# Kernel tuning notes

Measured on AMD Instinct MI355X. Metric: run time of the kernel, lower is better.

## Reference

```python
import jax, jax.numpy as jnp
import numpy as np

C_IN = 512


def _rms(h, gamma):
    # F.normalize(x, dim=1) * sqrt(C) * gamma  (channel_first, h: [b, c, l])
    c = h.shape[1]
    n = jnp.sqrt(jnp.sum(h * h, axis=1, keepdims=True))
    return h / jnp.maximum(n, 1e-12) * (c ** 0.5) * gamma[None, :, None]


def _pw(w, b, h):
    # 1x1 conv == pointwise linear over channel dim; h: [b, c, l]
    return jnp.einsum('oc,bcl->bol', w, h) + b[None, :, None]


def setup_inputs() -> dict:
    key = jax.random.key(0)
    ks = jax.random.split(key, 10)
    B, C, T, H, W = 1, C_IN, 16, 32, 32
    inp = {'x': jax.random.normal(ks[0], (B, C, T, H, W), jnp.float32)}
    names = ['qs', 'ks', 'vs', 'ps', 'qt', 'kt', 'vt', 'pt']
    for i, n in enumerate(names):
        inp[n + '_w'] = jax.random.normal(ks[i + 1], (C, C), jnp.float32) * 0.02
        inp[n + '_b'] = jnp.zeros((C,), jnp.float32)
    inp['norm_s_gamma'] = jnp.ones((C,), jnp.float32)
    inp['norm_t_gamma'] = jnp.ones((C,), jnp.float32)
    inp['max_temporal_window'] = 8
    return inp


def reference(x, qs_w, qs_b, ks_w, ks_b, vs_w, vs_b, ps_w, ps_b,
              qt_w, qt_b, kt_w, kt_b, vt_w, vt_b, pt_w, pt_b,
              norm_s_gamma, norm_t_gamma, max_temporal_window):
    B, C, T, H, W = x.shape
    scale = C ** -0.5

    # ---- spatial attention: (b t) c (h w) ----
    xs = x.transpose(0, 2, 1, 3, 4).reshape(B * T, C, H * W)
    h = _rms(xs, norm_s_gamma)
    q = _pw(qs_w, qs_b, h)
    k = _pw(ks_w, ks_b, h)
    v = _pw(vs_w, vs_b, h)
    scores = jnp.einsum('bcl,bcm->blm', q, k) * scale  # [bt, HW, HW]
    attn = jax.nn.softmax(scores, axis=-1)
    o = jnp.einsum('bcm,blm->bcl', v, attn)
    xs = xs + _pw(ps_w, ps_b, o)
    x = xs.reshape(B, T, C, H, W).transpose(0, 2, 1, 3, 4)

    # ---- temporal attention: (b h w) c t, causal + bounded window ----
    xt = x.transpose(0, 3, 4, 1, 2).reshape(B * H * W, C, T)
    h = _rms(xt, norm_t_gamma)
    q = _pw(qt_w, qt_b, h)
    k = _pw(kt_w, kt_b, h)
    v = _pw(vt_w, vt_b, h)
    scores = jnp.einsum('bcl,bcm->blm', q, k) * scale  # [bhw, T, T]
    i = jnp.arange(T)[:, None]
    j = jnp.arange(T)[None, :]
    allowed = j <= i  # causal
    if max_temporal_window is not None and max_temporal_window > 0:
        allowed = allowed & (i - j < max_temporal_window)  # sliding window
    mask = jnp.where(allowed, 0.0, jnp.finfo(scores.dtype).min)
    attn = jax.nn.softmax(scores + mask[None], axis=-1)
    o = jnp.einsum('bcm,blm->bcl', v, attn)
    xt = xt + _pw(pt_w, pt_b, o)
    x = xt.reshape(B, H, W, C, T).transpose(0, 3, 4, 1, 2)
    return x
```

## Files before the change

kernel.cpp:

```cpp
#include <hip/hip_runtime.h>

typedef __attribute__((ext_vector_type(8))) short bf16x8;
typedef __attribute__((ext_vector_type(4))) float f32x4;

__device__ __forceinline__ short f2bf(float f) {
  union { float f; unsigned u; } a; a.f = f;
  unsigned r = a.u + 0x7fffu + ((a.u >> 16) & 1u);
  return (short)(r >> 16);
}
__device__ __forceinline__ float bf2f(short s) {
  union { unsigned u; float f; } a;
  a.u = ((unsigned)(unsigned short)s) << 16; return a.f;
}
__device__ __forceinline__ float blo(unsigned u) { union { unsigned u; float f; } a; a.u = u << 16; return a.f; }
__device__ __forceinline__ float bhi(unsigned u) { union { unsigned u; float f; } a; a.u = u & 0xffff0000u; return a.f; }
__device__ __forceinline__ unsigned packbf(float lo, float hi) {
  return (unsigned)(unsigned short)f2bf(lo) | ((unsigned)(unsigned short)f2bf(hi) << 16);
}
__device__ __forceinline__ void ldscp16(const void* g, void* l) {
  __builtin_amdgcn_global_load_lds((const __attribute__((address_space(1))) void*)g,
                                   (__attribute__((address_space(3))) void*)l, 16, 0, 0);
}
__device__ __forceinline__ void stv(float* p, float v) { *p = v; }
__device__ __forceinline__ void stv(short* p, float v) { *p = f2bf(v); }

__global__ __launch_bounds__(256) void setup_all(
    const float* __restrict__ w0, const float* __restrict__ w1,
    const float* __restrict__ w2, const float* __restrict__ w3,
    const float* __restrict__ w4, const float* __restrict__ w5,
    const float* __restrict__ w6, const float* __restrict__ w7,
    const float* __restrict__ g_s, const float* __restrict__ g_t,
    short* __restrict__ Wb, float* __restrict__ zs,
    const float* __restrict__ qs_b, const float* __restrict__ vs_b,
    const float* __restrict__ ps_b, const float* __restrict__ qt_b,
    const float* __restrict__ vt_b, const float* __restrict__ pt_b,
    float* __restrict__ bt_s, float* __restrict__ bt_t,
    float* __restrict__ wus, float* __restrict__ wut) {
  const int bid = blockIdx.x, tid = threadIdx.x;
  if (bid < 8192) {
    int idx = bid * 256 + tid;
    const float* ws[8] = {w0, w1, w2, w3, w4, w5, w6, w7};
    int wi = idx >> 18, loc = idx & 262143;
    int r = loc >> 9, q = loc & 511;
    float v, g;
    if (wi == 3 || wi == 7) { v = ws[wi][loc]; g = 1.f; }
    else {
      v = ws[wi][q * 512 + r];
      g = (wi <= 2) ? g_s[r] : g_t[r];
    }
    Wb[idx] = f2bf(v * g);
  } else if (bid < 8512) {
    zs[(bid - 8192) * 256 + tid] = 0.f;
  } else {
    const int w = tid >> 6, lane = tid & 63;
    const int b = (bid - 8512) * 4 + w;
    float s = 0.f;
    if (b < 1024) {
      const bool sp = b < 512;
      const float* W = sp ? w3 : w7;
      const float* vb = sp ? vs_b : vt_b;
      const int r = b & 511;
#pragma unroll
      for (int c = lane; c < 512; c += 64) s += W[r * 512 + c] * vb[c];
#pragma unroll
      for (int off = 32; off > 0; off >>= 1) s += __shfl_xor(s, off);
      if (lane == 0) (sp ? bt_s : bt_t)[r] = s + (sp ? ps_b : pt_b)[r];
    } else {
      const bool sp = b < 1536;
      const float* W = sp ? w1 : w5;
      const float* qb = sp ? qs_b : qt_b;
      const int c = b & 511;
#pragma unroll
      for (int o = lane; o < 512; o += 64) s += W[o * 512 + c] * qb[o];
#pragma unroll
      for (int off = 32; off > 0; off >>= 1) s += __shfl_xor(s, off);
      if (lane == 0)
        (sp ? wus : wut)[c] = s * (sp ? g_s[c] : g_t[c]);
    }
  }
}

__global__ __launch_bounds__(256) void txp_sumsq(
    const float* __restrict__ src, short* __restrict__ dst,
    short* __restrict__ xb, float* __restrict__ ss,
    const float* __restrict__ wu, float* __restrict__ us) {
  constexpr long N = 16384;
  __shared__ short T[64][66];
  __shared__ float part[16][16][4];
  __shared__ float part2[16][16][4];
  const int tid = threadIdx.x;
  const long n0 = (long)blockIdx.x * 64;
  const int c0 = blockIdx.y * 64;
  const int n4 = (tid & 15) * 4;
  float s0 = 0.f, s1 = 0.f, s2 = 0.f, s3 = 0.f;
  float u0 = 0.f, u1 = 0.f, u2 = 0.f, u3 = 0.f;
#pragma unroll
  for (int i = 0; i < 4; ++i) {
    int cl = i * 16 + (tid >> 4);
    float4 v = *(const float4*)&src[(long)(c0 + cl) * N + n0 + n4];
    float wc = wu[c0 + cl];
    s0 += v.x * v.x; s1 += v.y * v.y; s2 += v.z * v.z; s3 += v.w * v.w;
    u0 += wc * v.x; u1 += wc * v.y; u2 += wc * v.z; u3 += wc * v.w;
    short e0 = f2bf(v.x), e1 = f2bf(v.y), e2 = f2bf(v.z), e3 = f2bf(v.w);
    T[n4 + 0][cl] = e0; T[n4 + 1][cl] = e1;
    T[n4 + 2][cl] = e2; T[n4 + 3][cl] = e3;
    uint2 o;
    o.x = (unsigned)(unsigned short)e0 | ((unsigned)(unsigned short)e1 << 16);
    o.y = (unsigned)(unsigned short)e2 | ((unsigned)(unsigned short)e3 << 16);
    *(uint2*)&xb[(long)(c0 + cl) * N + n0 + n4] = o;
  }
  part[tid >> 4][tid & 15][0] = s0; part[tid >> 4][tid & 15][1] = s1;
  part[tid >> 4][tid & 15][2] = s2; part[tid >> 4][tid & 15][3] = s3;
  part2[tid >> 4][tid & 15][0] = u0; part2[tid >> 4][tid & 15][1] = u1;
  part2[tid >> 4][tid & 15][2] = u2; part2[tid >> 4][tid & 15][3] = u3;
  __syncthreads();
  if (tid < 64) {
    float s = 0.f, u = 0.f;
#pragma unroll
    for (int cg = 0; cg < 16; ++cg) {
      s += part[cg][tid >> 2][tid & 3];
      u += part2[cg][tid >> 2][tid & 3];
    }
    atomicAdd(&ss[n0 + tid], s);
    atomicAdd(&us[n0 + tid], u);
  }
#pragma unroll
  for (int p = 0; p < 4; ++p) {
    int nl = p * 16 + (tid >> 4);
    int cl = (tid & 15) * 4;
    uint2 o;
    o.x = (unsigned)(unsigned short)T[nl][cl] |
          ((unsigned)(unsigned short)T[nl][cl + 1] << 16);
    o.y = (unsigned)(unsigned short)T[nl][cl + 2] |
          ((unsigned)(unsigned short)T[nl][cl + 3] << 16);
    *(uint2*)&dst[(n0 + nl) * 512 + c0 + cl] = o;
  }
}

template <typename OutT, int BIAS_MODE, int SCALE_MODE, int RESID_MODE, int EPI,
          int BM = 128, int FOLD = 0, int BK = 64, int SWZ = 0>
__global__ __launch_bounds__(256, 4) void gemm_nt(
    const short* __restrict__ A, const short* __restrict__ B,
    OutT* __restrict__ D, const float* __restrict__ bias,
    const float* __restrict__ ssv, const float* __restrict__ uvec,
    float* __restrict__ rs, float* __restrict__ rs2,
    const float* __restrict__ wvec,
    const float* __restrict__ residf, const short* __restrict__ residb,
    int K, int lda, int ldb, int ldd,
    long aBatch, long bBatch, long dBatch, long sBatch, float scale) {
  constexpr int WR = BM / 64;
  constexpr int WC = 4 / WR;
  constexpr int NW = (128 / WC) / 16;
  constexpr int CH = BK / 8;
  constexpr int MSK = CH - 1;
  constexpr int RPR = 256 / CH;
  __shared__ short As[BM * BK];
  __shared__ short Bs[128 * BK];
  const int tid = threadIdx.x;

  int lin = blockIdx.x + gridDim.x * (blockIdx.y + gridDim.y * blockIdx.z);
  if (SWZ) {
    const int nwg = gridDim.x * gridDim.y * gridDim.z;
    const int q = nwg >> 3, r = nwg & 7;
    const int xcd = lin & 7, idx = lin >> 3;
    lin = (xcd < r ? xcd * (q + 1) : r * (q + 1) + (xcd - r) * q) + idx;
  }
  const int bx = lin % gridDim.x;
  const int t1 = lin / gridDim.x;
  const int by = t1 % gridDim.y;
  const int bz = t1 / gridDim.y;

  const long i0 = (long)bx * BM;
  const long j0 = (long)by * 128;
  long aOff, bOff;
  if (FOLD) {
    aOff = 262144L * (bz < 2 ? 3 + 4 * bz : 4 * (bz - 2));
    bOff = 262144L * (bz < 2 ? 2 + 4 * bz : 1 + 4 * (bz - 2));
  } else {
    aOff = bz * aBatch; bOff = bz * bBatch;
  }
  const short* Ab = A + aOff + i0 * lda;
  const short* Bb = B + bOff + j0 * ldb;
  const int srow = tid / CH, scol = tid & MSK;
  const int lane = tid & 63;
  const int waveid = tid >> 6;
  const int wr = (waveid / WC) * 64;
  const int wc = (waveid % WC) * 64;
  const int quad = lane >> 4, l15 = lane & 15;

  f32x4 acc[4][NW] = {};

  for (int k0 = 0; k0 < K; k0 += BK) {
    __syncthreads();
#pragma unroll
    for (int p = 0; p < BM / RPR; ++p) {
      int row = p * RPR + srow;
      int gc = (scol ^ (row & MSK)) << 3;
      ldscp16(Ab + (long)row * lda + k0 + gc, &As[p * 2048 + tid * 8]);
    }
#pragma unroll
    for (int p = 0; p < 128 / RPR; ++p) {
      int row = p * RPR + srow;
      int gc = (scol ^ (row & MSK)) << 3;
      ldscp16(Bb + (long)row * ldb + k0 + gc, &Bs[p * 2048 + tid * 8]);
    }
    __syncthreads();
#pragma unroll
    for (int kk = 0; kk < BK / 32; ++kk) {
      bf16x8 af[4], bfr[NW];
#pragma unroll
      for (int a = 0; a < 4; ++a) {
        int row = wr + a * 16 + l15;
        int g = kk * 4 + quad;
        af[a] = *(const bf16x8*)&As[row * BK + ((g ^ (row & MSK)) << 3)];
      }
#pragma unroll
      for (int b = 0; b < NW; ++b) {
        int row = wc + b * 16 + l15;
        int g = kk * 4 + quad;
        bfr[b] = *(const bf16x8*)&Bs[row * BK + ((g ^ (row & MSK)) << 3)];
      }
#pragma unroll
      for (int a = 0; a < 4; ++a)
#pragma unroll
        for (int b = 0; b < NW; ++b)
          acc[a][b] = __builtin_amdgcn_mfma_f32_16x16x32_bf16(af[a], bfr[b], acc[a][b], 0, 0, 0);
    }
  }

  const long Doff = bz * dBatch;
#pragma unroll
  for (int a = 0; a < 4; ++a) {
    const int rb = (int)i0 + wr + a * 16 + quad * 4;
    float rsc[4];
    if (SCALE_MODE == 1 || SCALE_MODE == 4) {
#pragma unroll
      for (int r = 0; r < 4; ++r)
        rsc[r] = 22.627416997969522f /
                 fmaxf(sqrtf(ssv[bz * sBatch + rb + r]), 1e-12f);
    }
    if (SCALE_MODE == 3) {
#pragma unroll
      for (int r = 0; r < 4; ++r)
        rsc[r] = 1.f / ssv[bz * sBatch + rb + r];
    }
    float rp1[4] = {0.f, 0.f, 0.f, 0.f};
    float rp2[4] = {0.f, 0.f, 0.f, 0.f};
#pragma unroll
    for (int b = 0; b < NW; ++b) {
      const int cc = (int)j0 + wc + b * 16 + l15;
      float csc = 1.f, uu = 0.f, wv = 0.f;
      if (SCALE_MODE == 2 || SCALE_MODE == 4)
        csc = 22.627416997969522f /
              fmaxf(sqrtf(ssv[bz * sBatch + cc]), 1e-12f);
      if (SCALE_MODE == 4) uu = uvec[bz * sBatch + cc];
      if (EPI == 3) wv = wvec[cc];
      uint2 rtv;
      if (RESID_MODE == 3)
        rtv = *(const uint2*)&residb[(long)cc * 512 + rb];
#pragma unroll
      for (int r = 0; r < 4; ++r) {
        float val;
        if (SCALE_MODE == 4) {
          val = __expf(scale * csc * (rsc[r] * acc[a][b][r] + uu));
          rp1[r] += val;
          val *= csc;
        } else {
          val = acc[a][b][r] * scale;
          if (SCALE_MODE == 1 || SCALE_MODE == 3) val *= rsc[r];
          if (SCALE_MODE == 2) val *= csc;
        }
        if (BIAS_MODE == 1) val += bias[rb + r];
        if (BIAS_MODE == 2) val += bias[cc];
        const long off = Doff + (long)(rb + r) * ldd + cc;
        if (RESID_MODE == 1) val += residf[off];
        if (RESID_MODE == 2) val += bf2f(residb[off]);
        if (RESID_MODE == 3) val += bf2f(((const short*)&rtv)[r]);
        stv(D + off, val);
        if (EPI == 3) { rp1[r] += val * val; rp2[r] += val * wv; }
      }
    }
    if (EPI == 1 || EPI == 3) {
#pragma unroll
      for (int r = 0; r < 4; ++r) {
        float s = rp1[r];
#pragma unroll
        for (int off = 1; off < 16; off <<= 1) s += __shfl_xor(s, off);
        if (l15 == 0) atomicAdd(&rs[bz * sBatch + rb + r], s);
      }
      if (EPI == 3) {
#pragma unroll
        for (int r = 0; r < 4; ++r) {
          float s = rp2[r];
#pragma unroll
          for (int off = 1; off < 16; off <<= 1) s += __shfl_xor(s, off);
          if (l15 == 0) atomicAdd(&rs2[bz * sBatch + rb + r], s);
        }
      }
    }
  }
}

__global__ __launch_bounds__(256) void temporal_attn_v5(
    const short* __restrict__ h2, const short* __restrict__ Tt,
    const float* __restrict__ ss, const float* __restrict__ ut,
    const int* __restrict__ wndp, short* __restrict__ o, float scale) {
  constexpr int RS = 520;
  __shared__ short hq[16 * RS];
  __shared__ short tk[16 * RS];
  __shared__ float Plds[16][17];
  const int tid = threadIdx.x;
  const int w = tid >> 6, lane = tid & 63;
  const int hw = blockIdx.x;
  const int wnd = *wndp;

#pragma unroll
  for (int i = 0; i < 8; ++i) {
    int ci = w * 8 + i;
    int t = ci & 15;
    const short* src = (ci < 16) ? h2 : Tt;
    short* dst = (ci < 16) ? hq : tk;
    ldscp16(src + (long)(t * 1024 + hw) * 512 + lane * 8,
            dst + t * RS + lane * 8);
  }
  const int c0 = lane * 8;
  uint4 vch[16];
#pragma unroll
  for (int tp = 0; tp < 16; ++tp)
    vch[tp] = *(const uint4*)(h2 + (long)(tp * 1024 + hw) * 512 + c0);
  __syncthreads();

  if (w == 0) {
    const int quad = lane >> 4, m = lane & 15;
    f32x4 sacc = {};
#pragma unroll
    for (int s = 0; s < 16; ++s) {
      bf16x8 aq = *(const bf16x8*)&hq[m * RS + quad * 8 + s * 32];
      bf16x8 bk = *(const bf16x8*)&tk[m * RS + quad * 8 + s * 32];
      sacc = __builtin_amdgcn_mfma_f32_16x16x32_bf16(aq, bk, sacc, 0, 0, 0);
    }
    const float rmsj = 22.627416997969522f /
                       fmaxf(sqrtf(ss[m * 1024 + hw]), 1e-12f);
    const float uj = ut[m * 1024 + hw];
#pragma unroll
    for (int r = 0; r < 4; ++r) {
      const int i = quad * 4 + r;
      const int j = m;
      const float rmsi = 22.627416997969522f /
                         fmaxf(sqrtf(ss[i * 1024 + hw]), 1e-12f);
      const bool allowed = (j <= i) && (wnd <= 0 || (i - j) < wnd);
      float val = allowed ? scale * (rmsi * rmsj * sacc[r] + rmsj * uj) : -1e30f;
      float mx = val;
#pragma unroll
      for (int off = 1; off < 16; off <<= 1) mx = fmaxf(mx, __shfl_xor(mx, off));
      float e = allowed ? __expf(val - mx) : 0.f;
      float sum = e;
#pragma unroll
      for (int off = 1; off < 16; off <<= 1) sum += __shfl_xor(sum, off);
      Plds[i][j] = (e / sum) * rmsj;
    }
  }
  __syncthreads();

#pragma unroll
  for (int r = 0; r < 4; ++r) {
    const int t = w * 4 + r;
    const int tlo = (wnd > 0 && t - wnd + 1 > 0) ? t - wnd + 1 : 0;
    float a0 = 0.f, a1 = 0.f, a2 = 0.f, a3 = 0.f,
          a4 = 0.f, a5 = 0.f, a6 = 0.f, a7 = 0.f;
#pragma unroll
    for (int tp = 0; tp < 16; ++tp) {
      const float p = (tp >= tlo && tp <= t) ? Plds[t][tp] : 0.f;
      const uint4 vv = vch[tp];
      a0 += p * blo(vv.x); a1 += p * bhi(vv.x);
      a2 += p * blo(vv.y); a3 += p * bhi(vv.y);
      a4 += p * blo(vv.z); a5 += p * bhi(vv.z);
      a6 += p * blo(vv.w); a7 += p * bhi(vv.w);
    }
    uint4 ov;
    ov.x = packbf(a0, a1); ov.y = packbf(a2, a3);
    ov.z = packbf(a4, a5); ov.w = packbf(a6, a7);
    *(uint4*)(o + (long)(t * 1024 + hw) * 512 + c0) = ov;
  }
}

extern "C" void kernel_launch(void* const* d_in, const int* in_sizes, int n_in,
                              void* d_out, int out_size, void* d_ws, size_t ws_size,
                              hipStream_t stream) {
  const float* x    = (const float*)d_in[0];
  const float* qs_w = (const float*)d_in[1];
  const float* qs_b = (const float*)d_in[2];
  const float* ks_w = (const float*)d_in[3];
  const float* ks_b = (const float*)d_in[4];
  const float* vs_w = (const float*)d_in[5];
  const float* vs_b = (const float*)d_in[6];
  const float* ps_w = (const float*)d_in[7];
  const float* ps_b = (const float*)d_in[8];
  const float* qt_w = (const float*)d_in[9];
  const float* qt_b = (const float*)d_in[10];
  const float* kt_w = (const float*)d_in[11];
  const float* kt_b = (const float*)d_in[12];
  const float* vt_w = (const float*)d_in[13];
  const float* vt_b = (const float*)d_in[14];
  const float* pt_w = (const float*)d_in[15];
  const float* pt_b = (const float*)d_in[16];
  const float* g_s  = (const float*)d_in[17];
  const float* g_t  = (const float*)d_in[18];
  const int*   wnd  = (const int*)d_in[19];
  float* out = (float*)d_out;
  (void)ks_b; (void)kt_b;

  char* w = (char*)d_ws;
  short* Wb   = (short*)(w);
  float* ss_s = (float*)(w + (4L << 20));
  float* ss_t = (float*)(w + (4L << 20) + (64 << 10));
  float* rsum = (float*)(w + (4L << 20) + (128 << 10));
  float* us   = (float*)(w + (4L << 20) + (192 << 10));
  float* ut   = (float*)(w + (4L << 20) + (256 << 10));
  float* bt_s = (float*)(w + (4L << 20) + (320 << 10));
  float* bt_t = (float*)(w + (4L << 20) + (324 << 10));
  float* wus  = (float*)(w + (4L << 20) + (328 << 10));
  float* wut  = (float*)(w + (4L << 20) + (332 << 10));
  short* WF   = (short*)(w + (4L << 20) + (512 << 10));
  short* Wpv  = WF;
  short* Mqk  = WF + 2 * 262144;
  short* hb   = (short*)(w + (8L << 20));
  short* Tb   = (short*)(w + (24L << 20));
  short* xb   = (short*)(w + (40L << 20));
  short* oT   = (short*)(w + (56L << 20));
  short* h2   = (short*)(w + (72L << 20));
  short* S    = (short*)(w + (88L << 20));
  (void)in_sizes; (void)n_in; (void)out_size; (void)ws_size;

  const float scale = 0.04419417382415922f;

  setup_all<<<9024, 256, 0, stream>>>(
      qs_w, ks_w, vs_w, ps_w, qt_w, kt_w, vt_w, pt_w, g_s, g_t, Wb, ss_s,
      qs_b, vs_b, ps_b, qt_b, vt_b, pt_b, bt_s, bt_t, wus, wut);
  gemm_nt<short, 0, 0, 0, 0, 128, 1, 64, 0><<<dim3(4, 4, 4), 256, 0, stream>>>(
      Wb, Wb, WF, nullptr, nullptr, nullptr, nullptr, nullptr, nullptr,
      nullptr, nullptr, 512, 512, 512, 512, 0, 0, 262144L, 0, 1.f);

  txp_sumsq<<<dim3(256, 8, 1), 256, 0, stream>>>(x, hb, xb, ss_s, wus, us);
  gemm_nt<short, 0, 0, 0, 0, 128, 0, 64, 1><<<dim3(128, 4, 1), 256, 0, stream>>>(
      hb, Mqk, Tb, nullptr, nullptr, nullptr, nullptr, nullptr, nullptr,
      nullptr, nullptr, 512, 512, 512, 512, 0, 0, 0, 0, 1.f);
  gemm_nt<short, 0, 4, 0, 1, 128, 0, 64, 1><<<dim3(8, 8, 16), 256, 0, stream>>>(
      hb, Tb, S, nullptr, ss_s, us, rsum, nullptr, nullptr, nullptr, nullptr,
      512, 512, 512, 1024,
      1024L * 512, 1024L * 512, 1024L * 1024, 1024, scale);
  gemm_nt<short, 0, 3, 0, 0, 128, 0, 64, 1><<<dim3(8, 4, 16), 256, 0, stream>>>(
      S, xb, oT, nullptr, rsum, nullptr, nullptr, nullptr, nullptr,
      nullptr, nullptr, 1024, 1024, 16384, 512,
      1024L * 1024, 1024L, 1024L * 512, 1024, 1.f);
  gemm_nt<short, 2, 0, 2, 3, 128, 0, 64, 1><<<dim3(128, 4, 1), 256, 0, stream>>>(
      oT, Wpv, h2, bt_s, nullptr, nullptr, ss_t, ut, wut, nullptr, hb,
      512, 512, 512, 512, 0, 0, 0, 1024, 1.f);

  gemm_nt<short, 0, 0, 0, 0, 128, 0, 64, 1><<<dim3(128, 4, 1), 256, 0, stream>>>(
      h2, Mqk + 262144, Tb, nullptr, nullptr, nullptr, nullptr, nullptr,
      nullptr, nullptr, nullptr, 512, 512, 512, 512, 0, 0, 0, 0, 1.f);
  temporal_attn_v5<<<1024, 256, 0, stream>>>(h2, Tb, ss_t, ut, wnd, oT, scale);
  gemm_nt<float, 1, 0, 3, 0, 128, 0, 64, 1><<<dim3(4, 128, 1), 256, 0, stream>>>(
      Wpv + 262144, oT, out, bt_t, nullptr, nullptr, nullptr, nullptr,
      nullptr, nullptr, h2, 512, 512, 512, 16384, 0, 0, 0, 0, 1.f);
}
```

Measured before the change: 301.3 us.

## Fuse spatial attention score GEMM and PV GEMM into one flash-style kernel

```diff
diff --git a/kernel.cpp b/kernel.cpp
--- a/kernel.cpp
+++ b/kernel.cpp
@@ -233,7 +233,7 @@
   for (int a = 0; a < 4; ++a) {
     const int rb = (int)i0 + wr + a * 16 + quad * 4;
     float rsc[4];
-    if (SCALE_MODE == 1 || SCALE_MODE == 4) {
+    if (SCALE_MODE == 1) {
 #pragma unroll
       for (int r = 0; r < 4; ++r)
         rsc[r] = 22.627416997969522f /
@@ -249,27 +249,19 @@
 #pragma unroll
     for (int b = 0; b < NW; ++b) {
       const int cc = (int)j0 + wc + b * 16 + l15;
-      float csc = 1.f, uu = 0.f, wv = 0.f;
-      if (SCALE_MODE == 2 || SCALE_MODE == 4)
+      float csc = 1.f, wv = 0.f;
+      if (SCALE_MODE == 2)
         csc = 22.627416997969522f /
               fmaxf(sqrtf(ssv[bz * sBatch + cc]), 1e-12f);
-      if (SCALE_MODE == 4) uu = uvec[bz * sBatch + cc];
       if (EPI == 3) wv = wvec[cc];
       uint2 rtv;
       if (RESID_MODE == 3)
         rtv = *(const uint2*)&residb[(long)cc * 512 + rb];
 #pragma unroll
       for (int r = 0; r < 4; ++r) {
-        float val;
-        if (SCALE_MODE == 4) {
-          val = __expf(scale * csc * (rsc[r] * acc[a][b][r] + uu));
-          rp1[r] += val;
-          val *= csc;
-        } else {
-          val = acc[a][b][r] * scale;
-          if (SCALE_MODE == 1 || SCALE_MODE == 3) val *= rsc[r];
-          if (SCALE_MODE == 2) val *= csc;
-        }
+        float val = acc[a][b][r] * scale;
+        if (SCALE_MODE == 1 || SCALE_MODE == 3) val *= rsc[r];
+        if (SCALE_MODE == 2) val *= csc;
         if (BIAS_MODE == 1) val += bias[rb + r];
         if (BIAS_MODE == 2) val += bias[cc];
         const long off = Doff + (long)(rb + r) * ldd + cc;
@@ -280,7 +272,7 @@
         if (EPI == 3) { rp1[r] += val * val; rp2[r] += val * wv; }
       }
     }
-    if (EPI == 1 || EPI == 3) {
+    if (EPI == 3) {
 #pragma unroll
       for (int r = 0; r < 4; ++r) {
         float s = rp1[r];
@@ -288,14 +280,135 @@
         for (int off = 1; off < 16; off <<= 1) s += __shfl_xor(s, off);
         if (l15 == 0) atomicAdd(&rs[bz * sBatch + rb + r], s);
       }
-      if (EPI == 3) {
-#pragma unroll
-        for (int r = 0; r < 4; ++r) {
-          float s = rp2[r];
-#pragma unroll
-          for (int off = 1; off < 16; off <<= 1) s += __shfl_xor(s, off);
-          if (l15 == 0) atomicAdd(&rs2[bz * sBatch + rb + r], s);
-        }
+#pragma unroll
+      for (int r = 0; r < 4; ++r) {
+        float s = rp2[r];
+#pragma unroll
+        for (int off = 1; off < 16; off <<= 1) s += __shfl_xor(s, off);
+        if (l15 == 0) atomicAdd(&rs2[bz * sBatch + rb + r], s);
+      }
+    }
+  }
+}
+
+__global__ __launch_bounds__(512, 2) void fused_spatial(
+    const short* __restrict__ hb, const short* __restrict__ Tb,
+    const short* __restrict__ xb, const float* __restrict__ ss,
+    const float* __restrict__ us, short* __restrict__ oT, float scale) {
+  __shared__ short Kl[2][32 * 512];
+  __shared__ short Vl[2][512 * 32];
+  __shared__ short Pl[64 * 40];
+  __shared__ float rsl[64];
+  const int tid = threadIdx.x;
+  const int lane = tid & 63, w = tid >> 6;
+  const int quad = lane >> 4, l15 = lane & 15;
+
+  int lin = blockIdx.x + (blockIdx.y << 4);
+  { int idx = lin >> 3, xcd = lin & 7; lin = xcd * 32 + idx; }
+  const int qt = lin & 15, z = lin >> 4;
+  const long nbase = (long)z * 1024;
+  const int q0 = qt * 64;
+
+  const int band = w & 3, mh = w >> 2;
+  const int qh = w >> 2, ch = w & 3;
+
+  bf16x8 qreg[16];
+  {
+    const short* qrow = hb + (nbase + q0 + band * 16 + l15) * 512;
+#pragma unroll
+    for (int kk = 0; kk < 16; ++kk)
+      qreg[kk] = *(const bf16x8*)&qrow[kk * 32 + quad * 8];
+  }
+  float rsc[4];
+#pragma unroll
+  for (int rr = 0; rr < 4; ++rr)
+    rsc[rr] = 22.627416997969522f /
+              fmaxf(sqrtf(ss[nbase + q0 + band * 16 + quad * 4 + rr]), 1e-12f);
+  if (tid < 64) rsl[tid] = 0.f;
+
+  auto stageK = [&](int buf, int m0) {
+#pragma unroll
+    for (int p = 0; p < 4; ++p) {
+      int idx = p * 512 + tid;
+      int m = idx >> 6, c = idx & 63;
+      ldscp16(Tb + (nbase + m0 + m) * 512 + ((c ^ m) << 3), &Kl[buf][idx * 8]);
+    }
+  };
+  auto stageV = [&](int buf, int m0) {
+#pragma unroll
+    for (int p = 0; p < 4; ++p) {
+      int idx = p * 512 + tid;
+      int c = idx >> 2, c2 = idx & 3;
+      ldscp16(xb + (long)c * 16384 + nbase + m0 + ((c2 ^ (c & 3)) << 3),
+              &Vl[buf][idx * 8]);
+    }
+  };
+  stageK(0, 0); stageV(0, 0);
+  __syncthreads();
+
+  f32x4 acc[2][8] = {};
+  int cur = 0;
+  for (int t = 0; t < 32; ++t) {
+    const int m0 = t * 32;
+    if (t + 1 < 32) { stageK(cur ^ 1, m0 + 32); stageV(cur ^ 1, m0 + 32); }
+    f32x4 sacc = {};
+    {
+      const short* Kb = &Kl[cur][0];
+      const int row = mh * 16 + l15;
+#pragma unroll
+      for (int kk = 0; kk < 16; ++kk) {
+        int g = kk * 4 + quad;
+        bf16x8 kf = *(const bf16x8*)&Kb[row * 512 + ((g ^ row) << 3)];
+        sacc = __builtin_amdgcn_mfma_f32_16x16x32_bf16(qreg[kk], kf, sacc, 0, 0, 0);
+      }
+    }
+    {
+      const int gm = m0 + mh * 16 + l15;
+      const float csc = 22.627416997969522f /
+                        fmaxf(sqrtf(ss[nbase + gm]), 1e-12f);
+      const float uu = us[nbase + gm];
+#pragma unroll
+      for (int rr = 0; rr < 4; ++rr) {
+        float val = __expf(scale * csc * (rsc[rr] * sacc[rr] + uu));
+        Pl[(band * 16 + quad * 4 + rr) * 40 + mh * 16 + l15] = f2bf(val * csc);
+        float s = val;
+#pragma unroll
+        for (int off = 1; off < 16; off <<= 1) s += __shfl_xor(s, off);
+        if (l15 == 0) atomicAdd(&rsl[band * 16 + quad * 4 + rr], s);
+      }
+    }
+    __syncthreads();
+    {
+      const short* Vb = &Vl[cur][0];
+      bf16x8 pf[2];
+#pragma unroll
+      for (int a = 0; a < 2; ++a) {
+        int prow = qh * 32 + a * 16 + l15;
+        pf[a] = *(const bf16x8*)&Pl[prow * 40 + quad * 8];
+      }
+#pragma unroll
+      for (int b = 0; b < 8; ++b) {
+        int c = ch * 128 + b * 16 + l15;
+        bf16x8 vf = *(const bf16x8*)&Vb[c * 32 + ((quad ^ (c & 3)) << 3)];
+#pragma unroll
+        for (int a = 0; a < 2; ++a)
+          acc[a][b] = __builtin_amdgcn_mfma_f32_16x16x32_bf16(pf[a], vf, acc[a][b], 0, 0, 0);
+      }
+    }
+    __syncthreads();
+    cur ^= 1;
+  }
+#pragma unroll
+  for (int a = 0; a < 2; ++a) {
+    const int rowb = qh * 32 + a * 16 + quad * 4;
+#pragma unroll
+    for (int rr = 0; rr < 4; ++rr) {
+      const float inv = 1.f / rsl[rowb + rr];
+      const long n = nbase + q0 + rowb + rr;
+#pragma unroll
+      for (int b = 0; b < 8; ++b) {
+        const int c = ch * 128 + b * 16 + l15;
+        oT[n * 512 + c] = f2bf(acc[a][b][rr] * inv);
       }
     }
   }
@@ -429,7 +542,7 @@
   short* xb   = (short*)(w + (40L << 20));
   short* oT   = (short*)(w + (56L << 20));
   short* h2   = (short*)(w + (72L << 20));
-  short* S    = (short*)(w + (88L << 20));
+  (void)rsum;
   (void)in_sizes; (void)n_in; (void)out_size; (void)ws_size;
 
   const float scale = 0.04419417382415922f;
@@ -445,14 +558,8 @@
   gemm_nt<short, 0, 0, 0, 0, 128, 0, 64, 1><<<dim3(128, 4, 1), 256, 0, stream>>>(
       hb, Mqk, Tb, nullptr, nullptr, nullptr, nullptr, nullptr, nullptr,
       nullptr, nullptr, 512, 512, 512, 512, 0, 0, 0, 0, 1.f);
-  gemm_nt<short, 0, 4, 0, 1, 128, 0, 64, 1><<<dim3(8, 8, 16), 256, 0, stream>>>(
-      hb, Tb, S, nullptr, ss_s, us, rsum, nullptr, nullptr, nullptr, nullptr,
-      512, 512, 512, 1024,
-      1024L * 512, 1024L * 512, 1024L * 1024, 1024, scale);
-  gemm_nt<short, 0, 3, 0, 0, 128, 0, 64, 1><<<dim3(8, 4, 16), 256, 0, stream>>>(
-      S, xb, oT, nullptr, rsum, nullptr, nullptr, nullptr, nullptr,
-      nullptr, nullptr, 1024, 1024, 16384, 512,
-      1024L * 1024, 1024L, 1024L * 512, 1024, 1.f);
+  fused_spatial<<<dim3(16, 16), 512, 0, stream>>>(
+      hb, Tb, xb, ss_s, us, oT, scale);
   gemm_nt<short, 2, 0, 2, 3, 128, 0, 64, 1><<<dim3(128, 4, 1), 256, 0, stream>>>(
       oT, Wpv, h2, bt_s, nullptr, nullptr, ss_t, ut, wut, nullptr, hb,
       512, 512, 512, 512, 0, 0, 0, 1024, 1.f);
```

After: 319.0 us. 5.9% more time.

## Add 8-wave triple-buffered GEMM with async LDS prefetch for main GEMMs

Applied to the files above, without the earlier changes.

```diff
diff --git a/kernel.cpp b/kernel.cpp
--- a/kernel.cpp
+++ b/kernel.cpp
@@ -137,17 +137,10 @@
   }
 }
 
-template <typename OutT, int BIAS_MODE, int SCALE_MODE, int RESID_MODE, int EPI,
-          int BM = 128, int FOLD = 0, int BK = 64, int SWZ = 0>
+template <typename OutT, int BM = 128, int FOLD = 0, int BK = 64>
 __global__ __launch_bounds__(256, 4) void gemm_nt(
     const short* __restrict__ A, const short* __restrict__ B,
-    OutT* __restrict__ D, const float* __restrict__ bias,
-    const float* __restrict__ ssv, const float* __restrict__ uvec,
-    float* __restrict__ rs, float* __restrict__ rs2,
-    const float* __restrict__ wvec,
-    const float* __restrict__ residf, const short* __restrict__ residb,
-    int K, int lda, int ldb, int ldd,
-    long aBatch, long bBatch, long dBatch, long sBatch, float scale) {
+    OutT* __restrict__ D, int K, int lda, int ldb, int ldd, float scale) {
   constexpr int WR = BM / 64;
   constexpr int WC = 4 / WR;
   constexpr int NW = (128 / WC) / 16;
@@ -157,27 +150,15 @@
   __shared__ short As[BM * BK];
   __shared__ short Bs[128 * BK];
   const int tid = threadIdx.x;
-
-  int lin = blockIdx.x + gridDim.x * (blockIdx.y + gridDim.y * blockIdx.z);
-  if (SWZ) {
-    const int nwg = gridDim.x * gridDim.y * gridDim.z;
-    const int q = nwg >> 3, r = nwg & 7;
-    const int xcd = lin & 7, idx = lin >> 3;
-    lin = (xcd < r ? xcd * (q + 1) : r * (q + 1) + (xcd - r) * q) + idx;
-  }
-  const int bx = lin % gridDim.x;
-  const int t1 = lin / gridDim.x;
-  const int by = t1 % gridDim.y;
-  const int bz = t1 / gridDim.y;
-
-  const long i0 = (long)bx * BM;
-  const long j0 = (long)by * 128;
+  const int bz = blockIdx.z;
+  const long i0 = (long)blockIdx.x * BM;
+  const long j0 = (long)blockIdx.y * 128;
   long aOff, bOff;
   if (FOLD) {
     aOff = 262144L * (bz < 2 ? 3 + 4 * bz : 4 * (bz - 2));
     bOff = 262144L * (bz < 2 ? 2 + 4 * bz : 1 + 4 * (bz - 2));
   } else {
-    aOff = bz * aBatch; bOff = bz * bBatch;
+    aOff = 0; bOff = 0;
   }
   const short* Ab = A + aOff + i0 * lda;
   const short* Bb = B + bOff + j0 * ldb;
@@ -228,6 +209,121 @@
     }
   }
 
+  const long Doff = (long)bz * 262144L;
+#pragma unroll
+  for (int a = 0; a < 4; ++a) {
+    const int rb = (int)i0 + wr + a * 16 + quad * 4;
+#pragma unroll
+    for (int b = 0; b < NW; ++b) {
+      const int cc = (int)j0 + wc + b * 16 + l15;
+#pragma unroll
+      for (int r = 0; r < 4; ++r)
+        stv(D + Doff + (long)(rb + r) * ldd + cc, acc[a][b][r] * scale);
+    }
+  }
+}
+
+template <typename OutT, int BIAS_MODE, int SCALE_MODE, int RESID_MODE, int EPI,
+          int BM, int BN, int SWZ>
+__global__ __launch_bounds__(512, 1) void gemm8(
+    const short* __restrict__ A, const short* __restrict__ B,
+    OutT* __restrict__ D, const float* __restrict__ bias,
+    const float* __restrict__ ssv, const float* __restrict__ uvec,
+    float* __restrict__ rs, float* __restrict__ rs2,
+    const float* __restrict__ wvec, const short* __restrict__ residb,
+    int K, int lda, int ldb, int ldd,
+    long aBatch, long bBatch, long dBatch, long sBatch, float scale) {
+  constexpr int WN = BN / 64;
+  constexpr int ACH = BM * 8;
+  __shared__ short As[3][BM * 64];
+  __shared__ short Bs[3][BN * 64];
+  const int tid = threadIdx.x;
+  const int lane = tid & 63, w = tid >> 6;
+  const int quad = lane >> 4, l15 = lane & 15;
+
+  int lin = blockIdx.x + gridDim.x * (blockIdx.y + gridDim.y * blockIdx.z);
+  if (SWZ) {
+    const int nwg = gridDim.x * gridDim.y * gridDim.z;
+    const int q = nwg >> 3, r = nwg & 7;
+    const int xcd = lin & 7, idx = lin >> 3;
+    lin = (xcd < r ? xcd * (q + 1) : r * (q + 1) + (xcd - r) * q) + idx;
+  }
+  const int bx = lin % gridDim.x;
+  const int t1 = lin / gridDim.x;
+  const int by = t1 % gridDim.y;
+  const int bz = t1 / gridDim.y;
+
+  const long i0 = (long)bx * BM;
+  const long j0 = (long)by * BN;
+  const short* Ab = A + bz * aBatch + i0 * lda;
+  const short* Bb = B + bz * bBatch + j0 * ldb;
+  const int wr = (w / WN) * 64;
+  const int wc = (w % WN) * 64;
+
+  f32x4 acc[4][4] = {};
+
+  auto stage1 = [&](int buf, int k0, int s) {
+    int idx = s * 512 + tid;
+    if (idx < ACH) {
+      int row = idx >> 3, c = idx & 7;
+      ldscp16(Ab + (long)row * lda + k0 + ((c ^ (row & 7)) << 3),
+              &As[buf][idx * 8]);
+    } else {
+      int j = idx - ACH;
+      int row = j >> 3, c = j & 7;
+      ldscp16(Bb + (long)row * ldb + k0 + ((c ^ (row & 7)) << 3),
+              &Bs[buf][j * 8]);
+    }
+  };
+
+  const int NT = K >> 6;
+#pragma unroll
+  for (int s = 0; s < 6; ++s) stage1(0, 0, s);
+  if (NT > 1)
+#pragma unroll
+    for (int s = 0; s < 6; ++s) stage1(1, 64, s);
+
+  for (int t = 0; t < NT; ++t) {
+    const int buf = t % 3;
+    if (t + 1 < NT) asm volatile("s_waitcnt vmcnt(6)" ::: "memory");
+    else            asm volatile("s_waitcnt vmcnt(0)" ::: "memory");
+    __builtin_amdgcn_s_barrier();
+    const short* Ar = As[buf];
+    const short* Br = Bs[buf];
+    const bool pre = (t + 2 < NT);
+    const int pbuf = (t + 2) % 3, pk = (t + 2) * 64;
+#pragma unroll
+    for (int p = 0; p < 4; ++p) {
+      const int kk = p >> 1, bh = p & 1;
+      bf16x8 af[4], bfr[2];
+#pragma unroll
+      for (int a = 0; a < 4; ++a) {
+        int row = wr + a * 16 + l15;
+        int g = kk * 4 + quad;
+        af[a] = *(const bf16x8*)&Ar[row * 64 + ((g ^ (row & 7)) << 3)];
+      }
+#pragma unroll
+      for (int b = 0; b < 2; ++b) {
+        int row = wc + (bh * 2 + b) * 16 + l15;
+        int g = kk * 4 + quad;
+        bfr[b] = *(const bf16x8*)&Br[row * 64 + ((g ^ (row & 7)) << 3)];
+      }
+      if (pre && p < 3) { stage1(pbuf, pk, 2 * p); stage1(pbuf, pk, 2 * p + 1); }
+      __builtin_amdgcn_s_barrier();
+      asm volatile("s_waitcnt lgkmcnt(0)" ::: "memory");
+      __builtin_amdgcn_s_setprio(1);
+#pragma unroll
+      for (int a = 0; a < 4; ++a) {
+        acc[a][bh * 2 + 0] = __builtin_amdgcn_mfma_f32_16x16x32_bf16(
+            af[a], bfr[0], acc[a][bh * 2 + 0], 0, 0, 0);
+        acc[a][bh * 2 + 1] = __builtin_amdgcn_mfma_f32_16x16x32_bf16(
+            af[a], bfr[1], acc[a][bh * 2 + 1], 0, 0, 0);
+      }
+      __builtin_amdgcn_s_setprio(0);
+      __builtin_amdgcn_s_barrier();
+    }
+  }
+
   const long Doff = bz * dBatch;
 #pragma unroll
   for (int a = 0; a < 4; ++a) {
@@ -247,10 +343,10 @@
     float rp1[4] = {0.f, 0.f, 0.f, 0.f};
     float rp2[4] = {0.f, 0.f, 0.f, 0.f};
 #pragma unroll
-    for (int b = 0; b < NW; ++b) {
+    for (int b = 0; b < 4; ++b) {
       const int cc = (int)j0 + wc + b * 16 + l15;
       float csc = 1.f, uu = 0.f, wv = 0.f;
-      if (SCALE_MODE == 2 || SCALE_MODE == 4)
+      if (SCALE_MODE == 4)
         csc = 22.627416997969522f /
               fmaxf(sqrtf(ssv[bz * sBatch + cc]), 1e-12f);
       if (SCALE_MODE == 4) uu = uvec[bz * sBatch + cc];
@@ -268,12 +364,10 @@
         } else {
           val = acc[a][b][r] * scale;
           if (SCALE_MODE == 1 || SCALE_MODE == 3) val *= rsc[r];
-          if (SCALE_MODE == 2) val *= csc;
         }
         if (BIAS_MODE == 1) val += bias[rb + r];
         if (BIAS_MODE == 2) val += bias[cc];
         const long off = Doff + (long)(rb + r) * ldd + cc;
-        if (RESID_MODE == 1) val += residf[off];
         if (RESID_MODE == 2) val += bf2f(residb[off]);
         if (RESID_MODE == 3) val += bf2f(((const short*)&rtv)[r]);
         stv(D + off, val);
@@ -437,31 +531,30 @@
   setup_all<<<9024, 256, 0, stream>>>(
       qs_w, ks_w, vs_w, ps_w, qt_w, kt_w, vt_w, pt_w, g_s, g_t, Wb, ss_s,
       qs_b, vs_b, ps_b, qt_b, vt_b, pt_b, bt_s, bt_t, wus, wut);
-  gemm_nt<short, 0, 0, 0, 0, 128, 1, 64, 0><<<dim3(4, 4, 4), 256, 0, stream>>>(
-      Wb, Wb, WF, nullptr, nullptr, nullptr, nullptr, nullptr, nullptr,
-      nullptr, nullptr, 512, 512, 512, 512, 0, 0, 262144L, 0, 1.f);
+  gemm_nt<short, 128, 1, 64><<<dim3(4, 4, 4), 256, 0, stream>>>(
+      Wb, Wb, WF, 512, 512, 512, 512, 1.f);
 
   txp_sumsq<<<dim3(256, 8, 1), 256, 0, stream>>>(x, hb, xb, ss_s, wus, us);
-  gemm_nt<short, 0, 0, 0, 0, 128, 0, 64, 1><<<dim3(128, 4, 1), 256, 0, stream>>>(
+  gemm8<short, 0, 0, 0, 0, 256, 128, 1><<<dim3(64, 4, 1), 512, 0, stream>>>(
       hb, Mqk, Tb, nullptr, nullptr, nullptr, nullptr, nullptr, nullptr,
-      nullptr, nullptr, 512, 512, 512, 512, 0, 0, 0, 0, 1.f);
-  gemm_nt<short, 0, 4, 0, 1, 128, 0, 64, 1><<<dim3(8, 8, 16), 256, 0, stream>>>(
-      hb, Tb, S, nullptr, ss_s, us, rsum, nullptr, nullptr, nullptr, nullptr,
+      nullptr, 512, 512, 512, 512, 0, 0, 0, 0, 1.f);
+  gemm8<short, 0, 4, 0, 1, 128, 256, 1><<<dim3(8, 4, 16), 512, 0, stream>>>(
+      hb, Tb, S, nullptr, ss_s, us, rsum, nullptr, nullptr, nullptr,
       512, 512, 512, 1024,
       1024L * 512, 1024L * 512, 1024L * 1024, 1024, scale);
-  gemm_nt<short, 0, 3, 0, 0, 128, 0, 64, 1><<<dim3(8, 4, 16), 256, 0, stream>>>(
-      S, xb, oT, nullptr, rsum, nullptr, nullptr, nullptr, nullptr,
-      nullptr, nullptr, 1024, 1024, 16384, 512,
+  gemm8<short, 0, 3, 0, 0, 128, 256, 1><<<dim3(8, 2, 16), 512, 0, stream>>>(
+      S, xb, oT, nullptr, rsum, nullptr, nullptr, nullptr, nullptr, nullptr,
+      1024, 1024, 16384, 512,
       1024L * 1024, 1024L, 1024L * 512, 1024, 1.f);
-  gemm_nt<short, 2, 0, 2, 3, 128, 0, 64, 1><<<dim3(128, 4, 1), 256, 0, stream>>>(
-      oT, Wpv, h2, bt_s, nullptr, nullptr, ss_t, ut, wut, nullptr, hb,
+  gemm8<short, 2, 0, 2, 3, 256, 128, 1><<<dim3(64, 4, 1), 512, 0, stream>>>(
+      oT, Wpv, h2, bt_s, nullptr, nullptr, ss_t, ut, wut, hb,
       512, 512, 512, 512, 0, 0, 0, 1024, 1.f);
 
-  gemm_nt<short, 0, 0, 0, 0, 128, 0, 64, 1><<<dim3(128, 4, 1), 256, 0, stream>>>(
+  gemm8<short, 0, 0, 0, 0, 256, 128, 1><<<dim3(64, 4, 1), 512, 0, stream>>>(
       h2, Mqk + 262144, Tb, nullptr, nullptr, nullptr, nullptr, nullptr,
-      nullptr, nullptr, nullptr, 512, 512, 512, 512, 0, 0, 0, 0, 1.f);
+      nullptr, nullptr, 512, 512, 512, 512, 0, 0, 0, 0, 1.f);
   temporal_attn_v5<<<1024, 256, 0, stream>>>(h2, Tb, ss_t, ut, wnd, oT, scale);
-  gemm_nt<float, 1, 0, 3, 0, 128, 0, 64, 1><<<dim3(4, 128, 1), 256, 0, stream>>>(
+  gemm8<float, 1, 0, 3, 0, 128, 256, 1><<<dim3(4, 64, 1), 512, 0, stream>>>(
       Wpv + 262144, oT, out, bt_t, nullptr, nullptr, nullptr, nullptr,
-      nullptr, nullptr, h2, 512, 512, 512, 16384, 0, 0, 0, 0, 1.f);
-}
+      nullptr, h2, 512, 512, 512, 16384, 0, 0, 0, 0, 1.f);
+}
```

Measured after the change: 330.7 us. +9.8%, slower.

## Add weight-stationary GEMM kernel keeping 64x512 weight slice in LDS

Applied to the files above, without the earlier changes.

```diff
diff --git a/kernel.cpp b/kernel.cpp
--- a/kernel.cpp
+++ b/kernel.cpp
@@ -296,6 +296,100 @@
           for (int off = 1; off < 16; off <<= 1) s += __shfl_xor(s, off);
           if (l15 == 0) atomicAdd(&rs2[bz * sBatch + rb + r], s);
         }
+      }
+    }
+  }
+}
+
+template <typename OutT, int BIAS_MODE, int RESID_MODE, int EPI, int STREAM_A>
+__global__ __launch_bounds__(256, 2) void gemm_ws(
+    const short* __restrict__ Sm,
+    const short* __restrict__ St,
+    OutT* __restrict__ D, const float* __restrict__ bias,
+    float* __restrict__ rs, float* __restrict__ rs2,
+    const float* __restrict__ wvec, const short* __restrict__ residb,
+    int ldd) {
+  __shared__ short Ps[64 * 512];
+  const int tid = threadIdx.x;
+  const int lane = tid & 63, w = tid >> 6;
+  const int quad = lane >> 4, l15 = lane & 15;
+
+  int lin = blockIdx.x + (blockIdx.y << 3);
+  { int idx = lin >> 3, xcd = lin & 7; lin = xcd * 64 + idx; }
+  const int bx = lin & 7, by = lin >> 3;
+  const int p0 = bx * 64;
+  const long s0 = (long)by * 256;
+
+#pragma unroll
+  for (int i = 0; i < 16; ++i) {
+    int idx = i * 256 + tid;
+    int r = idx >> 6, c = idx & 63;
+    ldscp16(Sm + (p0 + r) * 512 + ((c ^ (r & 7)) << 3), &Ps[idx * 8]);
+  }
+  __syncthreads();
+
+  const long sbase = s0 + w * 64;
+  f32x4 acc[4][4] = {};
+#pragma unroll
+  for (int kk = 0; kk < 16; ++kk) {
+    bf16x8 gf[4], lf[4];
+#pragma unroll
+    for (int a = 0; a < 4; ++a)
+      gf[a] = *(const bf16x8*)&St[(sbase + a * 16 + l15) * 512 + kk * 32 + quad * 8];
+#pragma unroll
+    for (int b = 0; b < 4; ++b) {
+      int pr = b * 16 + l15;
+      lf[b] = *(const bf16x8*)&Ps[pr * 512 + (((kk * 4 + quad) ^ (pr & 7)) << 3)];
+    }
+#pragma unroll
+    for (int a = 0; a < 4; ++a)
+#pragma unroll
+      for (int b = 0; b < 4; ++b)
+        acc[a][b] = __builtin_amdgcn_mfma_f32_16x16x32_bf16(
+            STREAM_A ? gf[a] : lf[a], STREAM_A ? lf[b] : gf[b], acc[a][b], 0, 0, 0);
+  }
+
+  const int rbase = STREAM_A ? (int)sbase : p0;
+  const int cbase = STREAM_A ? p0 : (int)sbase;
+#pragma unroll
+  for (int a = 0; a < 4; ++a) {
+    const int rb = rbase + a * 16 + quad * 4;
+    float rp1[4] = {0.f, 0.f, 0.f, 0.f};
+    float rp2[4] = {0.f, 0.f, 0.f, 0.f};
+#pragma unroll
+    for (int b = 0; b < 4; ++b) {
+      const int cc = cbase + b * 16 + l15;
+      float wv = 0.f;
+      if (EPI == 3) wv = wvec[cc];
+      uint2 rtv;
+      if (RESID_MODE == 3)
+        rtv = *(const uint2*)&residb[(long)cc * 512 + rb];
+#pragma unroll
+      for (int r = 0; r < 4; ++r) {
+        float val = acc[a][b][r];
+        if (BIAS_MODE == 1) val += bias[rb + r];
+        if (BIAS_MODE == 2) val += bias[cc];
+        const long off = (long)(rb + r) * ldd + cc;
+        if (RESID_MODE == 2) val += bf2f(residb[off]);
+        if (RESID_MODE == 3) val += bf2f(((const short*)&rtv)[r]);
+        stv(D + off, val);
+        if (EPI == 3) { rp1[r] += val * val; rp2[r] += val * wv; }
+      }
+    }
+    if (EPI == 3) {
+#pragma unroll
+      for (int r = 0; r < 4; ++r) {
+        float s = rp1[r];
+#pragma unroll
+        for (int off = 1; off < 16; off <<= 1) s += __shfl_xor(s, off);
+        if (l15 == 0) atomicAdd(&rs[rb + r], s);
+      }
+#pragma unroll
+      for (int r = 0; r < 4; ++r) {
+        float s = rp2[r];
+#pragma unroll
+        for (int off = 1; off < 16; off <<= 1) s += __shfl_xor(s, off);
+        if (l15 == 0) atomicAdd(&rs2[rb + r], s);
       }
     }
   }
@@ -442,9 +536,8 @@
       nullptr, nullptr, 512, 512, 512, 512, 0, 0, 262144L, 0, 1.f);
 
   txp_sumsq<<<dim3(256, 8, 1), 256, 0, stream>>>(x, hb, xb, ss_s, wus, us);
-  gemm_nt<short, 0, 0, 0, 0, 128, 0, 64, 1><<<dim3(128, 4, 1), 256, 0, stream>>>(
-      hb, Mqk, Tb, nullptr, nullptr, nullptr, nullptr, nullptr, nullptr,
-      nullptr, nullptr, 512, 512, 512, 512, 0, 0, 0, 0, 1.f);
+  gemm_ws<short, 0, 0, 0, 1><<<dim3(8, 64), 256, 0, stream>>>(
+      Mqk, hb, Tb, nullptr, nullptr, nullptr, nullptr, nullptr, 512);
   gemm_nt<short, 0, 4, 0, 1, 128, 0, 64, 1><<<dim3(8, 8, 16), 256, 0, stream>>>(
       hb, Tb, S, nullptr, ss_s, us, rsum, nullptr, nullptr, nullptr, nullptr,
       512, 512, 512, 1024,
@@ -453,15 +546,12 @@
       S, xb, oT, nullptr, rsum, nullptr, nullptr, nullptr, nullptr,
       nullptr, nullptr, 1024, 1024, 16384, 512,
       1024L * 1024, 1024L, 1024L * 512, 1024, 1.f);
-  gemm_nt<short, 2, 0, 2, 3, 128, 0, 64, 1><<<dim3(128, 4, 1), 256, 0, stream>>>(
-      oT, Wpv, h2, bt_s, nullptr, nullptr, ss_t, ut, wut, nullptr, hb,
-      512, 512, 512, 512, 0, 0, 0, 1024, 1.f);
-
-  gemm_nt<short, 0, 0, 0, 0, 128, 0, 64, 1><<<dim3(128, 4, 1), 256, 0, stream>>>(
-      h2, Mqk + 262144, Tb, nullptr, nullptr, nullptr, nullptr, nullptr,
-      nullptr, nullptr, nullptr, 512, 512, 512, 512, 0, 0, 0, 0, 1.f);
+  gemm_ws<short, 2, 2, 3, 1><<<dim3(8, 64), 256, 0, stream>>>(
+      Wpv, oT, h2, bt_s, ss_t, ut, wut, hb, 512);
+
+  gemm_ws<short, 0, 0, 0, 1><<<dim3(8, 64), 256, 0, stream>>>(
+      Mqk + 262144, h2, Tb, nullptr, nullptr, nullptr, nullptr, nullptr, 512);
   temporal_attn_v5<<<1024, 256, 0, stream>>>(h2, Tb, ss_t, ut, wnd, oT, scale);
-  gemm_nt<float, 1, 0, 3, 0, 128, 0, 64, 1><<<dim3(4, 128, 1), 256, 0, stream>>>(
-      Wpv + 262144, oT, out, bt_t, nullptr, nullptr, nullptr, nullptr,
-      nullptr, nullptr, h2, 512, 512, 512, 16384, 0, 0, 0, 0, 1.f);
-}
+  gemm_ws<float, 1, 3, 0, 0><<<dim3(8, 64), 256, 0, stream>>>(
+      Wpv + 262144, oT, out, bt_t, nullptr, nullptr, nullptr, h2, 16384);
+}
```

Measured after the change: 317.4 us. 5.4% more time.
